# Kernel optimization log

Hardware: AMD Instinct MI355X
Metric: run time of the kernel (lower is better)

Reference implementation:

```python
import jax, jax.numpy as jnp
import numpy as np

N, M = 16384, 12
OA, OB = 92, 41
AF, BF = 128, 64
LD, NC, B = 2, 3, 128


def _bn(x, g, b):
    # training-mode BatchNorm1d over all leading dims (biased variance), eps=1e-5
    x2 = x.reshape(-1, x.shape[-1])
    m = x2.mean(0)
    v = x2.var(0)
    return (x - m) * jax.lax.rsqrt(v + 1e-5) * g + b


def _conv(atom, nbr, idx, Wa, Wb, g1a, b1a, g1b, b1b, g2a, b2a):
    n, m = idx.shape
    # gather neighbor atom features and concat [self, neighbor, bond] -> [N,M,2A+Bf]
    total = jnp.concatenate([jnp.broadcast_to(atom[:, None, :], (n, m, atom.shape[1])), atom[idx], nbr], axis=2)
    ga = _bn(jnp.einsum('nmi,io->nmo', total, Wa), g1a, b1a)
    af, ac = jnp.split(ga, 2, axis=2)
    asum = _bn(jnp.sum(jax.nn.sigmoid(af) * jax.nn.softplus(ac), axis=1), g2a, b2a)
    out1 = jax.nn.softplus(atom + asum)
    gb = _bn(jnp.einsum('nmi,io->nmo', total, Wb), g1b, b1b)
    bf, bc = jnp.split(gb, 2, axis=2)
    out2 = jax.nn.softplus(nbr + jax.nn.sigmoid(bf) * jax.nn.softplus(bc))
    return out1, out2


def _forward(atom_fea, nbr_fea, emb_atom_W, emb_atom_b, emb_bond_W, emb_bond_b,
             emb_atom2_W, emb_atom2_b, emb_bond2_W, emb_bond2_b,
             mu_W, mu_b, logvar_W, logvar_b, dec_W, dec_b,
             c1_Wa, c1_Wb, c1_g1a, c1_b1a, c1_g1b, c1_b1b, c1_g2a, c1_b2a,
             c2_Wa, c2_Wb, c2_g1a, c2_b1a, c2_g1b, c2_b1b, c2_g2a, c2_b2a,
             nbr_fea_idx, num_crystals):
    n, m = nbr_fea_idx.shape
    a_per = n // num_crystals
    anbr = atom_fea[nbr_fea_idx]  # [N,M,OA]
    total_input_fea = jnp.concatenate([jnp.broadcast_to(atom_fea[:, None, :], anbr.shape), anbr, nbr_fea], axis=2)
    a = atom_fea @ emb_atom_W + emb_atom_b            # [N,AF]
    nb = nbr_fea @ emb_bond_W + emb_bond_b            # [N,M,BF]
    for i in range(NC):
        a, nb = _conv(a, nb, nbr_fea_idx, c1_Wa[i], c1_Wb[i], c1_g1a[i], c1_b1a[i], c1_g1b[i], c1_b1b[i], c1_g2a[i], c1_b2a[i])
    non_pooled = jnp.concatenate([a, nb.reshape(n, -1)], axis=1)  # [N, AF+M*BF]
    # equal-size contiguous crystals -> pooling = reshape + mean
    pa = jax.nn.softplus(a.reshape(num_crystals, a_per, -1).mean(1))
    pn = jax.nn.softplus(nb.reshape(num_crystals, a_per, m, -1).mean(1)).reshape(num_crystals, -1)
    pooled = jnp.concatenate([pa, pn], axis=1)        # [B, AF+M*BF]
    mu = pooled @ mu_W + mu_b
    logvar = pooled @ logvar_W + logvar_b
    eps = jax.random.normal(jax.random.key(42), mu.shape, mu.dtype)  # fixed reparam noise
    z = mu + eps * jnp.exp(0.5 * logvar)
    zd = z @ dec_W + dec_b                            # [B, AF+M*BF]
    dec = jax.nn.softplus((non_pooled.reshape(num_crystals, a_per, -1) * zd[:, None, :] / pooled[:, None, :]).reshape(n, -1))
    za = dec[:, :AF]
    dn = dec[:, AF:].reshape(n, m, BF)
    for i in range(NC):
        za, dn = _conv(za, dn, nbr_fea_idx, c2_Wa[i], c2_Wb[i], c2_g1a[i], c2_b1a[i], c2_g1b[i], c2_b1b[i], c2_g2a[i], c2_b2a[i])
    za = jax.nn.sigmoid(za @ emb_atom2_W + emb_atom2_b)   # [N,OA]
    dn = jax.nn.sigmoid(dn @ emb_bond2_W + emb_bond2_b)   # [N,M,OB]
    znbr = za[nbr_fea_idx]
    z_dec = jnp.concatenate([jnp.broadcast_to(za[:, None, :], znbr.shape), znbr, dn], axis=2)  # [N,M,2*OA+OB]
    return z_dec, mu, logvar, z, total_input_fea


def setup_inputs() -> dict:
    key = jax.random.key(0)
    def nrm(i, shape, s=0.05):
        return (jax.random.normal(jax.random.fold_in(key, i), shape) * s).astype(jnp.float32)
    inp = {
        'atom_fea': nrm(0, (N, OA), 1.0),
        'nbr_fea': nrm(1, (N, M, OB), 1.0),
        'nbr_fea_idx': jax.random.randint(jax.random.fold_in(key, 2), (N, M), 0, N),
        'num_crystals': B,
        'emb_atom_W': nrm(3, (OA, AF)), 'emb_atom_b': jnp.zeros((AF,), jnp.float32),
        'emb_bond_W': nrm(4, (OB, BF)), 'emb_bond_b': jnp.zeros((BF,), jnp.float32),
        'emb_atom2_W': nrm(5, (AF, OA)), 'emb_atom2_b': jnp.zeros((OA,), jnp.float32),
        'emb_bond2_W': nrm(6, (BF, OB)), 'emb_bond2_b': jnp.zeros((OB,), jnp.float32),
        'mu_W': nrm(7, (AF + M * BF, LD)), 'mu_b': jnp.zeros((LD,), jnp.float32),
        'logvar_W': nrm(8, (AF + M * BF, LD)), 'logvar_b': jnp.zeros((LD,), jnp.float32),
        'dec_W': nrm(9, (LD, AF + M * BF)), 'dec_b': jnp.zeros((AF + M * BF,), jnp.float32),
        'c1_Wa': nrm(10, (NC, 2 * AF + BF, 2 * AF)), 'c1_Wb': nrm(11, (NC, 2 * AF + BF, 2 * BF)),
        'c1_g1a': jnp.ones((NC, 2 * AF), jnp.float32), 'c1_b1a': jnp.zeros((NC, 2 * AF), jnp.float32),
        'c1_g1b': jnp.ones((NC, 2 * BF), jnp.float32), 'c1_b1b': jnp.zeros((NC, 2 * BF), jnp.float32),
        'c1_g2a': jnp.ones((NC, AF), jnp.float32), 'c1_b2a': jnp.zeros((NC, AF), jnp.float32),
        'c2_Wa': nrm(12, (NC, 2 * AF + BF, 2 * AF)), 'c2_Wb': nrm(13, (NC, 2 * AF + BF, 2 * BF)),
        'c2_g1a': jnp.ones((NC, 2 * AF), jnp.float32), 'c2_b1a': jnp.zeros((NC, 2 * AF), jnp.float32),
        'c2_g1b': jnp.ones((NC, 2 * BF), jnp.float32), 'c2_b1b': jnp.zeros((NC, 2 * BF), jnp.float32),
        'c2_g2a': jnp.ones((NC, AF), jnp.float32), 'c2_b2a': jnp.zeros((NC, AF), jnp.float32),
    }
    return inp


def reference(atom_fea, nbr_fea, nbr_fea_idx, num_crystals,
              emb_atom_W, emb_atom_b, emb_bond_W, emb_bond_b,
              emb_atom2_W, emb_atom2_b, emb_bond2_W, emb_bond2_b,
              mu_W, mu_b, logvar_W, logvar_b, dec_W, dec_b,
              c1_Wa, c1_Wb, c1_g1a, c1_b1a, c1_g1b, c1_b1b, c1_g2a, c1_b2a,
              c2_Wa, c2_Wb, c2_g1a, c2_b1a, c2_g1b, c2_b1b, c2_g2a, c2_b2a):
    return _forward(atom_fea, nbr_fea, emb_atom_W, emb_atom_b, emb_bond_W, emb_bond_b,
                    emb_atom2_W, emb_atom2_b, emb_bond2_W, emb_bond2_b,
                    mu_W, mu_b, logvar_W, logvar_b, dec_W, dec_b,
                    c1_Wa, c1_Wb, c1_g1a, c1_b1a, c1_g1b, c1_b1b, c1_g2a, c1_b2a,
                    c2_Wa, c2_Wb, c2_g1a, c2_b1a, c2_g1b, c2_b1b, c2_g2a, c2_b2a,
                    nbr_fea_idx, num_crystals)
```

## Files before the change

kernel.cpp:

```cpp
#include <hip/hip_runtime.h>
#include <hip/hip_bf16.h>
#include <hip/hip_fp16.h>
#include <cstdint>
#include <cstddef>

#define N_ATOM 16384
#define M_NBR  12
#define NCRY   128
#define NM     (N_ATOM*M_NBR)

#define O_ZDEC 0
#define O_MU   44236800
#define O_LV   44237056
#define O_Z    44237312
#define O_TIF  44237568

typedef unsigned short ushort_t;
typedef float f32x4 __attribute__((ext_vector_type(4)));
typedef short bf16x8 __attribute__((ext_vector_type(8)));
typedef unsigned int u32x4 __attribute__((ext_vector_type(4)));

__device__ __forceinline__ float sigmoidf_(float x){
  return __fdividef(1.f, 1.f + __expf(-x));
}
__device__ __forceinline__ float softplusf_(float x){
  return fmaxf(x,0.f) + 0.69314718056f * __log2f(1.f + __expf(-fabsf(x)));
}
__device__ __forceinline__ uint32_t rotl32_(uint32_t x, int r){ return (x<<r)|(x>>(32-r)); }
__device__ __forceinline__ float bf2f(ushort_t u){ return __uint_as_float(((uint32_t)u)<<16); }
__device__ __forceinline__ ushort_t f2bf(float x){
  uint32_t u = __float_as_uint(x);
  uint32_t r = (u + 0x7FFFu + ((u>>16)&1u)) >> 16;
  return (ushort_t)r;
}

#define GLDS16(g, l) __builtin_amdgcn_global_load_lds( \
    (const __attribute__((address_space(1))) void*)(g), \
    (__attribute__((address_space(3))) void*)(l), 16, 0, 0)

__global__ void gen_eps_kernel(float* __restrict__ eps){
  int j = threadIdx.x;
  const uint32_t k0 = 0u, k1 = 42u;
  const uint32_t ks2 = k0 ^ k1 ^ 0x1BD11BDAu;
  uint32_t x0 = 0u + k0;
  uint32_t x1 = (uint32_t)j + k1;
#define RND_(r) { x0 += x1; x1 = rotl32_(x1, r); x1 ^= x0; }
  RND_(13) RND_(15) RND_(26) RND_(6)  x0 += k1;  x1 += ks2 + 1u;
  RND_(17) RND_(29) RND_(16) RND_(24) x0 += ks2; x1 += k0 + 2u;
  RND_(13) RND_(15) RND_(26) RND_(6)  x0 += k0;  x1 += k1 + 3u;
  RND_(17) RND_(29) RND_(16) RND_(24) x0 += k1;  x1 += ks2 + 4u;
  RND_(13) RND_(15) RND_(26) RND_(6)  x0 += ks2; x1 += k0 + 5u;
#undef RND_
  uint32_t bits = x0 ^ x1;
  float f = __uint_as_float((bits >> 9) | 0x3f800000u) - 1.0f;
  float u = __fadd_rn(__fmul_rn(f, 1.99999994f), -0.99999994f);
  u = fmaxf(-0.99999994f, u);
  float w = -log1pf(-u*u);
  float p;
  if (w < 5.0f){
    w -= 2.5f;
    p = 2.81022636e-08f;
    p = fmaf(p, w, 3.43273939e-07f);
    p = fmaf(p, w, -3.5233877e-06f);
    p = fmaf(p, w, -4.39150654e-06f);
    p = fmaf(p, w, 0.00021858087f);
    p = fmaf(p, w, -0.00125372503f);
    p = fmaf(p, w, -0.00417768164f);
    p = fmaf(p, w, 0.246640727f);
    p = fmaf(p, w, 1.50140941f);
  } else {
    w = sqrtf(w) - 3.0f;
    p = -0.000200214257f;
    p = fmaf(p, w, 0.000100950558f);
    p = fmaf(p, w, 0.00134934322f);
    p = fmaf(p, w, -0.00367342844f);
    p = fmaf(p, w, 0.00573950773f);
    p = fmaf(p, w, -0.0076224613f);
    p = fmaf(p, w, 0.00943887047f);
    p = fmaf(p, w, 1.00167406f);
    p = fmaf(p, w, 2.83297682f);
  }
  eps[j] = 1.41421356237f * (p * u);
}

__global__ void tif_v2(const float* __restrict__ atom, const float* __restrict__ nbr,
                       const int* __restrict__ idx, float* __restrict__ out){
  int e0 = blockIdx.x*2048 + threadIdx.x;
#pragma unroll
  for (int i=0;i<8;++i){
    int e = e0 + i*256;
    int r = e/225, c = e - r*225;
    float v;
    if (c < 92)       v = atom[(r/12)*92 + c];
    else if (c < 184) v = atom[idx[r]*92 + (c-92)];
    else              v = nbr[(size_t)r*41 + (c-184)];
    __builtin_nontemporal_store(v, out + (size_t)e);
  }
}

__global__ void embed_atom_kernel(const float* __restrict__ atom, const float* __restrict__ W,
                                  const float* __restrict__ bias, ushort_t* __restrict__ a0){
  __shared__ float row[92];
  int i = blockIdx.x; int t = threadIdx.x;
  if (t < 92) row[t] = atom[i*92+t];
  __syncthreads();
  float s = bias[t];
#pragma unroll
  for (int k=0;k<92;++k) s = fmaf(row[k], W[k*128+t], s);
  a0[(size_t)i*128+t] = f2bf(s);
}

__global__ void embed_bond_kernel(const float* __restrict__ nbr, const float* __restrict__ W,
                                  const float* __restrict__ bias, ushort_t* __restrict__ nb0){
  __shared__ float rows[4][41];
  int r0 = blockIdx.x*4; int t = threadIdx.x;
  if (t < 164) rows[t/41][t%41] = nbr[(size_t)r0*41 + t];
  __syncthreads();
  int rr = t >> 6, c = t & 63;
  float s = bias[c];
#pragma unroll
  for (int k=0;k<41;++k) s = fmaf(rows[rr][k], W[k*64+c], s);
  nb0[(size_t)(r0+rr)*64 + c] = f2bf(s);
}

__global__ void wtr2_kernel(const float* __restrict__ Wa, const float* __restrict__ Wb,
                            ushort_t* __restrict__ Wt, float* __restrict__ zstats){
  __shared__ ushort_t tile[32][33];
  if (blockIdx.x == 0 && blockIdx.y == 0){
#pragma unroll
    for (int k=0;k<4;++k) zstats[threadIdx.x + k*256] = 0.f;
  }
  int by = blockIdx.y;
  const float* W; int NO, o0, obase;
  if (by < 8){ W = Wa; NO = 256; o0 = by*32; obase = o0; }
  else       { W = Wb; NO = 128; o0 = (by-8)*32; obase = 256 + o0; }
  int k0 = blockIdx.x*32;
  int tx = threadIdx.x & 31, ty = threadIdx.x >> 5;
#pragma unroll
  for (int i = ty; i < 32; i += 8)
    tile[i][tx] = f2bf(W[(size_t)(k0+i)*NO + o0 + tx]);
  __syncthreads();
#pragma unroll
  for (int i = ty; i < 32; i += 8)
    Wt[(size_t)(obase+i)*320 + k0 + tx] = tile[tx][i];
}

#define GEMM_LDS_V9 75776
__launch_bounds__(256, 2)
__global__ void conv_gemm_v9(const ushort_t* __restrict__ a_bf, const ushort_t* __restrict__ nb_bf,
                             const int* __restrict__ idx, const ushort_t* __restrict__ Wt,
                             __half* __restrict__ O, float* __restrict__ sums){
  extern __shared__ char smraw[];
  ushort_t* sm   = (ushort_t*)smraw;
  float*   sqred = (float*)(smraw + 73728);
  int*     idxs  = (int*)(smraw + 74752);
  ushort_t* As = sm;
  ushort_t* Bs = sm + 24576;
  const int t = threadIdx.x;
  const int lane = t & 63;
  const int w = t >> 6;
  const int lm = lane & 15, lg = lane >> 4;
  const int row0 = blockIdx.x * 256;
  const int cb   = blockIdx.y;
  const int col0 = cb * 128;
  __half* Ob = O + (size_t)cb * ((size_t)NM*128);

  idxs[t] = idx[row0 + t];
  sqred[t] = 0.f;

  auto stage = [&](int ks, int b_){
    ushort_t* Ad = As + b_*8192;
    ushort_t* Bd = Bs + b_*4096;
#pragma unroll
    for (int i=0;i<4;++i){
      int e = t + i*256;
      int r = e >> 2, ch = e & 3;
      const ushort_t* ga;
      if (ks < 4)      ga = a_bf + (size_t)((row0+r)/12)*128 + ks*32 + ch*8;
      else if (ks < 8) ga = a_bf + (size_t)idxs[r]*128 + (ks-4)*32 + ch*8;
      else             ga = nb_bf + (size_t)(row0+r)*64 + (ks-8)*32 + ch*8;
      GLDS16(ga, Ad + e*8);
    }
#pragma unroll
    for (int i=0;i<2;++i){
      int e = t + i*256;
      int r = e >> 2, ch = e & 3;
      GLDS16(Wt + (size_t)(col0+r)*320 + ks*32 + ch*8, Bd + e*8);
    }
  };

  stage(0, 0);
  stage(1, 1);

  f32x4 acc[4][8] = {};
#pragma unroll
  for (int ks = 0; ks < 10; ++ks){
    const int buf = ks % 3;
    if (ks < 8){
      stage(ks+2, (ks+2) % 3);
      asm volatile("s_waitcnt vmcnt(12)" ::: "memory");
    } else if (ks == 8){
      asm volatile("s_waitcnt vmcnt(6)" ::: "memory");
    } else {
      asm volatile("s_waitcnt vmcnt(0)" ::: "memory");
    }
    __builtin_amdgcn_s_barrier();
    __builtin_amdgcn_sched_barrier(0);
    const ushort_t* Ab = As + buf*8192;
    const ushort_t* Bb = Bs + buf*4096;
    bf16x8 afr[4], bfr[8];
#pragma unroll
    for (int fm=0; fm<4; ++fm)
      afr[fm] = *(const bf16x8*)&Ab[(w*64 + fm*16 + lm)*32 + lg*8];
#pragma unroll
    for (int fn=0; fn<8; ++fn)
      bfr[fn] = *(const bf16x8*)&Bb[(fn*16 + lm)*32 + lg*8];
    __builtin_amdgcn_s_setprio(1);
#pragma unroll
    for (int fm=0; fm<4; ++fm)
#pragma unroll
      for (int fn=0; fn<8; ++fn)
        acc[fm][fn] = __builtin_amdgcn_mfma_f32_16x16x32_bf16(afr[fm], bfr[fn], acc[fm][fn], 0, 0, 0);
    __builtin_amdgcn_s_setprio(0);
    asm volatile("s_waitcnt lgkmcnt(0)" ::: "memory");
    __builtin_amdgcn_sched_barrier(0);
    __builtin_amdgcn_s_barrier();
  }

#pragma unroll
  for (int fm=0; fm<4; ++fm){
    int rw = w*64 + fm*16 + lg*4;
#pragma unroll
    for (int fn=0; fn<8; ++fn){
      int cl = fn*16 + lm;
#pragma unroll
      for (int j=0; j<4; ++j){
        __half h = __float2half(acc[fm][fn][j]);
        sm[(rw+j)*136 + cl] = *(ushort_t*)&h;
      }
    }
  }
  __syncthreads();

  const int cch = t & 15, rb = t >> 4;
  float s1[8] = {0.f,0.f,0.f,0.f,0.f,0.f,0.f,0.f};
  float s2[8] = {0.f,0.f,0.f,0.f,0.f,0.f,0.f,0.f};
#pragma unroll
  for (int i=0; i<16; ++i){
    int row = rb + i*16;
    u32x4 v = *(const u32x4*)&sm[row*136 + cch*8];
    __builtin_nontemporal_store(v, (u32x4*)(Ob + (size_t)(row0+row)*128 + cch*8));
    const __half* hp = (const __half*)&v;
#pragma unroll
    for (int k=0;k<8;++k){
      float f = __half2float(hp[k]);
      s1[k] += f;
      s2[k] += f*f;
    }
  }
#pragma unroll
  for (int k=0;k<8;++k){
    atomicAdd(&sqred[cch*8+k], s1[k]);
    atomicAdd(&sqred[128+cch*8+k], s2[k]);
  }
  __syncthreads();
  if (t < 128){
    atomicAdd(&sums[col0 + t], sqred[t]);
    atomicAdd(&sums[384 + col0 + t], sqred[128+t]);
  }
}

__global__ void apply_gagb(const __half* __restrict__ O0, const __half* __restrict__ O1,
                           const __half* __restrict__ O2, ushort_t* __restrict__ nb,
                           const float* __restrict__ sums,
                           const float* __restrict__ g1a, const float* __restrict__ b1a,
                           const float* __restrict__ g1b, const float* __restrict__ b1b,
                           float* __restrict__ asum, float* __restrict__ st){
  __shared__ float red[256];
  int bx = blockIdx.x;
  int t = threadIdx.x;
  if (bx < 1024){
    red[t] = 0.f;
    int c8 = t & 15, al = t >> 4;
    int i = bx*16 + al;
    int c0 = c8*8;
    float gf[8], bfv[8], gc[8], bcv[8];
#pragma unroll
    for (int k=0;k<8;++k){
      int c = c0+k;
      float mf = sums[c]*(1.f/NM);
      float rf = rsqrtf(sums[384+c]*(1.f/NM) - mf*mf + 1e-5f);
      gf[k]  = g1a[c]*rf;      bfv[k] = b1a[c] - mf*gf[k];
      float mc = sums[c+128]*(1.f/NM);
      float rc = rsqrtf(sums[384+c+128]*(1.f/NM) - mc*mc + 1e-5f);
      gc[k]  = g1a[c+128]*rc;  bcv[k] = b1a[c+128] - mc*gc[k];
    }
    float s[8] = {0.f,0.f,0.f,0.f,0.f,0.f,0.f,0.f};
    size_t base = (size_t)i*12*128;
#pragma unroll
    for (int j=0;j<12;++j){
      u32x4 vf = __builtin_nontemporal_load((const u32x4*)(O0 + base + j*128 + c0));
      u32x4 vc = __builtin_nontemporal_load((const u32x4*)(O1 + base + j*128 + c0));
      const __half* hf = (const __half*)&vf;
      const __half* hc = (const __half*)&vc;
#pragma unroll
      for (int k=0;k<8;++k)
        s[k] += sigmoidf_(fmaf(__half2float(hf[k]), gf[k], bfv[k]))
              * softplusf_(fmaf(__half2float(hc[k]), gc[k], bcv[k]));
    }
    float* dst = asum + (size_t)i*128 + c0;
    __syncthreads();
#pragma unroll
    for (int k=0;k<8;++k){
      dst[k] = s[k];
      atomicAdd(&red[c0+k], s[k]);
      atomicAdd(&red[128+c0+k], s[k]*s[k]);
    }
    __syncthreads();
    atomicAdd(&st[t], red[t]);
  } else {
    int c8 = t & 7, rloc = t >> 3;
    int r = (bx-1024)*32 + rloc;
    int c0 = c8*8;
    float gf[8], bfv[8], gc[8], bcv[8];
#pragma unroll
    for (int k=0;k<8;++k){
      int c = c0+k;
      float mf = sums[256+c]*(1.f/NM);
      float rf = rsqrtf(sums[384+256+c]*(1.f/NM) - mf*mf + 1e-5f);
      gf[k]  = g1b[c]*rf;      bfv[k] = b1b[c] - mf*gf[k];
      float mc = sums[256+64+c]*(1.f/NM);
      float rc = rsqrtf(sums[384+256+64+c]*(1.f/NM) - mc*mc + 1e-5f);
      gc[k]  = g1b[c+64]*rc;   bcv[k] = b1b[c+64] - mc*gc[k];
    }
    size_t gbase = (size_t)r*128;
    u32x4 vf = __builtin_nontemporal_load((const u32x4*)(O2 + gbase + c0));
    u32x4 vc = __builtin_nontemporal_load((const u32x4*)(O2 + gbase + 64 + c0));
    const __half* hf = (const __half*)&vf;
    const __half* hc = (const __half*)&vc;
    ushort_t* np = nb + (size_t)r*64 + c0;
    u32x4 old = *(const u32x4*)np;
    const ushort_t* op = (const ushort_t*)&old;
    u32x4 outv;
    ushort_t* ov = (ushort_t*)&outv;
#pragma unroll
    for (int k=0;k<8;++k){
      float x = bf2f(op[k]) + sigmoidf_(fmaf(__half2float(hf[k]), gf[k], bfv[k]))
                            * softplusf_(fmaf(__half2float(hc[k]), gc[k], bcv[k]));
      ov[k] = f2bf(softplusf_(x));
    }
    *(u32x4*)np = outv;
  }
}

__global__ void out1_wtr(ushort_t* __restrict__ a0, const float* __restrict__ asum,
                         const float* __restrict__ st, const float* __restrict__ g2a,
                         const float* __restrict__ b2a,
                         const float* __restrict__ Wa_next, const float* __restrict__ Wb_next,
                         ushort_t* __restrict__ Wt, float* __restrict__ zstats){
  __shared__ ushort_t tile[32][33];
  int bx = blockIdx.x;
  int t = threadIdx.x;
  if (bx < 120){
    if (Wa_next == nullptr) return;
    int by = bx / 10, kx = bx - by*10;
    const float* W; int NO, o0, obase;
    if (by < 8){ W = Wa_next; NO = 256; o0 = by*32; obase = o0; }
    else       { W = Wb_next; NO = 128; o0 = (by-8)*32; obase = 256 + o0; }
    int k0 = kx*32;
    int tx = t & 31, ty = t >> 5;
#pragma unroll
    for (int i = ty; i < 32; i += 8)
      tile[i][tx] = f2bf(W[(size_t)(k0+i)*NO + o0 + tx]);
    __syncthreads();
#pragma unroll
    for (int i = ty; i < 32; i += 8)
      Wt[(size_t)(obase+i)*320 + k0 + tx] = tile[tx][i];
  } else if (bx == 120){
    if (Wa_next == nullptr) return;
#pragma unroll
    for (int k=0;k<4;++k) zstats[t + k*256] = 0.f;
  } else {
    int e = (bx-121)*256 + t;
    int c = e & 127;
    float m  = st[c]*(1.f/N_ATOM);
    float var = st[128+c]*(1.f/N_ATOM) - m*m;
    float rs = rsqrtf(var + 1e-5f);
    float g = g2a[c]*rs;
    float b = b2a[c] - m*g;
    a0[e] = f2bf(softplusf_(bf2f(a0[e]) + fmaf(asum[e], g, b)));
  }
}

__global__ void pool_a_kernel(const ushort_t* __restrict__ a, float* __restrict__ pooled){
  int b = blockIdx.x; int c = threadIdx.x;
  float s = 0.f;
  for (int i=0;i<128;++i) s += bf2f(a[(size_t)((b<<7)+i)*128 + c]);
  pooled[b*896 + c] = softplusf_(s * (1.f/128.f));
}

__launch_bounds__(768)
__global__ void pool_n_kernel(const ushort_t* __restrict__ nb, float* __restrict__ pooled){
  int b = blockIdx.x; int t = threadIdx.x;
  float s = 0.f;
  for (int i=0;i<128;++i) s += bf2f(nb[(size_t)((b<<7)+i)*768 + t]);
  pooled[b*896 + 128 + t] = softplusf_(s * (1.f/128.f));
}

__global__ void muz_kernel(const float* __restrict__ pooled, const float* __restrict__ muW,
                           const float* __restrict__ mub, const float* __restrict__ lvW,
                           const float* __restrict__ lvb, const float* __restrict__ eps,
                           float* __restrict__ out_mu, float* __restrict__ out_lv,
                           float* __restrict__ out_z, float* __restrict__ zws){
  int t = threadIdx.x;
  int b = t >> 1, l = t & 1;
  const float* pr = pooled + b*896;
  float smu = mub[l], slv = lvb[l];
  for (int k=0;k<896;++k){
    float p = pr[k];
    smu = fmaf(p, muW[k*2+l], smu);
    slv = fmaf(p, lvW[k*2+l], slv);
  }
  out_mu[t] = smu; out_lv[t] = slv;
  float zv = fmaf(eps[t], __expf(0.5f*slv), smu);
  out_z[t] = zv; zws[t] = zv;
}

__global__ void compute_f_kernel(const float* __restrict__ zws, const float* __restrict__ decW,
                                 const float* __restrict__ decb, const float* __restrict__ pooled,
                                 float* __restrict__ f){
  int b = blockIdx.x;
  float z0 = zws[b*2], z1 = zws[b*2+1];
  for (int k = threadIdx.x; k < 896; k += 256){
    float zd = fmaf(z0, decW[k], fmaf(z1, decW[896+k], decb[k]));
    f[b*896+k] = __fdividef(zd, pooled[b*896+k]);
  }
}

__global__ void dec_atom_kernel(ushort_t* __restrict__ a, const float* __restrict__ f){
  int e = blockIdx.x*256+threadIdx.x;
  int c = e & 127; int b = e >> 14;
  a[e] = f2bf(softplusf_(bf2f(a[e]) * f[b*896 + c]));
}

__global__ void dec_bond_kernel(ushort_t* __restrict__ nb, const float* __restrict__ f){
  int i = blockIdx.x; int off = blockIdx.y*256 + threadIdx.x;
  int b = i >> 7;
  size_t e = (size_t)i*768 + off;
  nb[e] = f2bf(softplusf_(bf2f(nb[e]) * f[b*896 + 128 + off]));
}

__global__ void embed_atom2_kernel(const ushort_t* __restrict__ a, const float* __restrict__ W,
                                   const float* __restrict__ bias, float* __restrict__ za2){
  __shared__ float row[128];
  int i = blockIdx.x; int t = threadIdx.x;
  row[t] = bf2f(a[(size_t)i*128+t]);
  __syncthreads();
  if (t < 92){
    float s = bias[t];
#pragma unroll
    for (int k=0;k<128;++k) s = fmaf(row[k], W[k*92+t], s);
    za2[(size_t)i*92+t] = sigmoidf_(s);
  }
}

__global__ void bproj_kernel(const ushort_t* __restrict__ nb, const float* __restrict__ W,
                             const float* __restrict__ bias, float* __restrict__ bp){
  __shared__ float Ws[64][41];
  __shared__ float rows[6][64];
  int t = threadIdx.x;
  for (int e=t; e<64*41; e+=256) Ws[e/41][e%41] = W[e];
  int r0 = blockIdx.x*6;
  for (int e=t; e<6*64; e+=256){
    int rr = e>>6, c = e&63;
    rows[rr][c] = bf2f(nb[(size_t)(r0+rr)*64 + c]);
  }
  __syncthreads();
  if (t < 246){
    int rr = t/41, o = t - rr*41;
    float s = bias[o];
#pragma unroll
    for (int k=0;k<64;++k) s = fmaf(rows[rr][k], Ws[k][o], s);
    bp[(size_t)(r0+rr)*41 + o] = sigmoidf_(s);
  }
}

__global__ void zdec_v2(const float* __restrict__ za2, const float* __restrict__ bp,
                        const int* __restrict__ idx, float* __restrict__ out){
  int e0 = blockIdx.x*2048 + threadIdx.x;
#pragma unroll
  for (int i=0;i<8;++i){
    int e = e0 + i*256;
    int r = e/225, c = e - r*225;
    float v;
    if (c < 92)       v = za2[(size_t)(r/12)*92 + c];
    else if (c < 184) v = za2[(size_t)idx[r]*92 + (c-92)];
    else              v = bp[(size_t)r*41 + (c-184)];
    __builtin_nontemporal_store(v, out + (size_t)e);
  }
}

struct WsPlan {
  ushort_t *Abf, *NBbf, *Wt;
  __half* big;
  float *asum, *pooled, *fbuf, *zws, *eps, *sums0, *sums1;
};

struct PassW {
  const float *Wa,*Wb,*g1a,*b1a,*g1b,*b1b,*g2a,*b2a;
};

extern "C" void kernel_launch(void* const* d_in, const int* in_sizes, int n_in,
                              void* d_out, int out_size, void* d_ws, size_t ws_size,
                              hipStream_t stream) {
  (void)in_sizes; (void)n_in; (void)out_size; (void)ws_size;
  const float* atom_fea   = (const float*)d_in[0];
  const float* nbr_fea    = (const float*)d_in[1];
  const int*   idx        = (const int*)d_in[2];
  const float* emb_atom_W = (const float*)d_in[4];
  const float* emb_atom_b = (const float*)d_in[5];
  const float* emb_bond_W = (const float*)d_in[6];
  const float* emb_bond_b = (const float*)d_in[7];
  const float* emb_atom2_W= (const float*)d_in[8];
  const float* emb_atom2_b= (const float*)d_in[9];
  const float* emb_bond2_W= (const float*)d_in[10];
  const float* emb_bond2_b= (const float*)d_in[11];
  const float* mu_W       = (const float*)d_in[12];
  const float* mu_b       = (const float*)d_in[13];
  const float* lv_W       = (const float*)d_in[14];
  const float* lv_b       = (const float*)d_in[15];
  const float* dec_W      = (const float*)d_in[16];
  const float* dec_b      = (const float*)d_in[17];
  const float* c1_Wa  = (const float*)d_in[18];
  const float* c1_Wb  = (const float*)d_in[19];
  const float* c1_g1a = (const float*)d_in[20];
  const float* c1_b1a = (const float*)d_in[21];
  const float* c1_g1b = (const float*)d_in[22];
  const float* c1_b1b = (const float*)d_in[23];
  const float* c1_g2a = (const float*)d_in[24];
  const float* c1_b2a = (const float*)d_in[25];
  const float* c2_Wa  = (const float*)d_in[26];
  const float* c2_Wb  = (const float*)d_in[27];
  const float* c2_g1a = (const float*)d_in[28];
  const float* c2_b1a = (const float*)d_in[29];
  const float* c2_g1b = (const float*)d_in[30];
  const float* c2_b1b = (const float*)d_in[31];
  const float* c2_g2a = (const float*)d_in[32];
  const float* c2_b2a = (const float*)d_in[33];

  float* out = (float*)d_out;

  hipFuncSetAttribute((const void*)conv_gemm_v9,
                      hipFuncAttributeMaxDynamicSharedMemorySize, GEMM_LDS_V9);

  WsPlan P;
  char* w = (char*)d_ws;
  auto alloc = [&](size_t bytes) -> char* {
    char* p = w; w += (bytes + 255) & ~(size_t)255; return p;
  };
  P.Abf    = (ushort_t*)alloc((size_t)N_ATOM*128*2);
  P.NBbf   = (ushort_t*)alloc((size_t)NM*64*2);
  P.big    = (__half*)  alloc((size_t)NM*384*2);
  P.asum   = (float*)   alloc((size_t)N_ATOM*128*4);
  P.pooled = (float*)   alloc(114688*4);
  P.fbuf   = (float*)   alloc(114688*4);
  P.Wt     = (ushort_t*)alloc(384*320*2);
  P.zws    = (float*)   alloc(256*4);
  P.eps    = (float*)   alloc(256*4);
  P.sums0  = (float*)   alloc(1024*4);
  P.sums1  = (float*)   alloc(1024*4);
  float* za2   = P.asum;
  float* bproj = (float*)P.big;

  PassW pw[6] = {
    { c1_Wa,            c1_Wb,            c1_g1a,       c1_b1a,       c1_g1b,       c1_b1b,       c1_g2a,       c1_b2a       },
    { c1_Wa+320*256,    c1_Wb+320*128,    c1_g1a+256,   c1_b1a+256,   c1_g1b+128,   c1_b1b+128,   c1_g2a+128,   c1_b2a+128   },
    { c1_Wa+2*320*256,  c1_Wb+2*320*128,  c1_g1a+2*256, c1_b1a+2*256, c1_g1b+2*128, c1_b1b+2*128, c1_g2a+2*128, c1_b2a+2*128 },
    { c2_Wa,            c2_Wb,            c2_g1a,       c2_b1a,       c2_g1b,       c2_b1b,       c2_g2a,       c2_b2a       },
    { c2_Wa+320*256,    c2_Wb+320*128,    c2_g1a+256,   c2_b1a+256,   c2_g1b+128,   c2_b1b+128,   c2_g2a+128,   c2_b2a+128   },
    { c2_Wa+2*320*256,  c2_Wb+2*320*128,  c2_g1a+2*256, c2_b1a+2*256, c2_g1b+2*128, c2_b1b+2*128, c2_g2a+2*128, c2_b2a+2*128 },
  };

  auto conv_pass = [&](int p){
    float* sums_cur = (p & 1) ? P.sums1 : P.sums0;
    float* sums_nxt = (p & 1) ? P.sums0 : P.sums1;
    const __half* O0 = P.big;
    const __half* O1 = P.big + (size_t)NM*128;
    const __half* O2 = P.big + (size_t)NM*256;
    conv_gemm_v9<<<dim3(NM/256, 3), 256, GEMM_LDS_V9, stream>>>(P.Abf, P.NBbf, idx, P.Wt, P.big, sums_cur);
    apply_gagb<<<7168, 256, 0, stream>>>(O0, O1, O2, P.NBbf, sums_cur,
                                         pw[p].g1a, pw[p].b1a, pw[p].g1b, pw[p].b1b,
                                         P.asum, sums_cur + 768);
    const float* Wa_n = (p < 5) ? pw[p+1].Wa : nullptr;
    const float* Wb_n = (p < 5) ? pw[p+1].Wb : nullptr;
    out1_wtr<<<8313, 256, 0, stream>>>(P.Abf, P.asum, sums_cur + 768,
                                       pw[p].g2a, pw[p].b2a, Wa_n, Wb_n, P.Wt, sums_nxt);
  };

  gen_eps_kernel<<<1, 256, 0, stream>>>(P.eps);
  tif_v2<<<21600, 256, 0, stream>>>(atom_fea, nbr_fea, idx, out + O_TIF);
  embed_atom_kernel<<<N_ATOM, 128, 0, stream>>>(atom_fea, emb_atom_W, emb_atom_b, P.Abf);
  embed_bond_kernel<<<NM/4, 256, 0, stream>>>(nbr_fea, emb_bond_W, emb_bond_b, P.NBbf);
  wtr2_kernel<<<dim3(10,12), 256, 0, stream>>>(pw[0].Wa, pw[0].Wb, P.Wt, P.sums0);

  conv_pass(0);
  conv_pass(1);
  conv_pass(2);

  pool_a_kernel<<<NCRY, 128, 0, stream>>>(P.Abf, P.pooled);
  pool_n_kernel<<<NCRY, 768, 0, stream>>>(P.NBbf, P.pooled);
  muz_kernel<<<1, 256, 0, stream>>>(P.pooled, mu_W, mu_b, lv_W, lv_b, P.eps,
                                    out + O_MU, out + O_LV, out + O_Z, P.zws);
  compute_f_kernel<<<NCRY, 256, 0, stream>>>(P.zws, dec_W, dec_b, P.pooled, P.fbuf);
  dec_atom_kernel<<<N_ATOM*128/256, 256, 0, stream>>>(P.Abf, P.fbuf);
  dim3 gdb(N_ATOM, 3);
  dec_bond_kernel<<<gdb, 256, 0, stream>>>(P.NBbf, P.fbuf);

  conv_pass(3);
  conv_pass(4);
  conv_pass(5);

  embed_atom2_kernel<<<N_ATOM, 128, 0, stream>>>(P.Abf, emb_atom2_W, emb_atom2_b, za2);
  bproj_kernel<<<NM/6, 256, 0, stream>>>(P.NBbf, emb_bond2_W, emb_bond2_b, bproj);
  zdec_v2<<<21600, 256, 0, stream>>>(za2, bproj, idx, out + O_ZDEC);
}
```

Before: 1.630 ms.

## Merge small launches and swizzle GEMM workgroup order for cache locality

Several independent small kernels are merged into single launches that branch on block index: atom and bond embedding, the two pooling kernels, and the two decoder scaling kernels. The eps generation is folded into the mu/z kernel. The conv GEMM moves from a 2D grid to a flat grid with a remapping that spreads consecutive workgroups across 8 groups, so row-tile/column-block pairs interleave differently. The aim is to cut launch overhead and improve L2 reuse of gathered rows. The remapping changes cache behaviour in ways that are hard to predict.

```diff
diff --git a/kernel.cpp b/kernel.cpp
--- a/kernel.cpp
+++ b/kernel.cpp
@@ -37,51 +37,6 @@
 #define GLDS16(g, l) __builtin_amdgcn_global_load_lds( \
     (const __attribute__((address_space(1))) void*)(g), \
     (__attribute__((address_space(3))) void*)(l), 16, 0, 0)
-
-__global__ void gen_eps_kernel(float* __restrict__ eps){
-  int j = threadIdx.x;
-  const uint32_t k0 = 0u, k1 = 42u;
-  const uint32_t ks2 = k0 ^ k1 ^ 0x1BD11BDAu;
-  uint32_t x0 = 0u + k0;
-  uint32_t x1 = (uint32_t)j + k1;
-#define RND_(r) { x0 += x1; x1 = rotl32_(x1, r); x1 ^= x0; }
-  RND_(13) RND_(15) RND_(26) RND_(6)  x0 += k1;  x1 += ks2 + 1u;
-  RND_(17) RND_(29) RND_(16) RND_(24) x0 += ks2; x1 += k0 + 2u;
-  RND_(13) RND_(15) RND_(26) RND_(6)  x0 += k0;  x1 += k1 + 3u;
-  RND_(17) RND_(29) RND_(16) RND_(24) x0 += k1;  x1 += ks2 + 4u;
-  RND_(13) RND_(15) RND_(26) RND_(6)  x0 += ks2; x1 += k0 + 5u;
-#undef RND_
-  uint32_t bits = x0 ^ x1;
-  float f = __uint_as_float((bits >> 9) | 0x3f800000u) - 1.0f;
-  float u = __fadd_rn(__fmul_rn(f, 1.99999994f), -0.99999994f);
-  u = fmaxf(-0.99999994f, u);
-  float w = -log1pf(-u*u);
-  float p;
-  if (w < 5.0f){
-    w -= 2.5f;
-    p = 2.81022636e-08f;
-    p = fmaf(p, w, 3.43273939e-07f);
-    p = fmaf(p, w, -3.5233877e-06f);
-    p = fmaf(p, w, -4.39150654e-06f);
-    p = fmaf(p, w, 0.00021858087f);
-    p = fmaf(p, w, -0.00125372503f);
-    p = fmaf(p, w, -0.00417768164f);
-    p = fmaf(p, w, 0.246640727f);
-    p = fmaf(p, w, 1.50140941f);
-  } else {
-    w = sqrtf(w) - 3.0f;
-    p = -0.000200214257f;
-    p = fmaf(p, w, 0.000100950558f);
-    p = fmaf(p, w, 0.00134934322f);
-    p = fmaf(p, w, -0.00367342844f);
-    p = fmaf(p, w, 0.00573950773f);
-    p = fmaf(p, w, -0.0076224613f);
-    p = fmaf(p, w, 0.00943887047f);
-    p = fmaf(p, w, 1.00167406f);
-    p = fmaf(p, w, 2.83297682f);
-  }
-  eps[j] = 1.41421356237f * (p * u);
-}
 
 __global__ void tif_v2(const float* __restrict__ atom, const float* __restrict__ nbr,
                        const int* __restrict__ idx, float* __restrict__ out){
@@ -98,29 +53,32 @@
   }
 }
 
-__global__ void embed_atom_kernel(const float* __restrict__ atom, const float* __restrict__ W,
-                                  const float* __restrict__ bias, ushort_t* __restrict__ a0){
-  __shared__ float row[92];
-  int i = blockIdx.x; int t = threadIdx.x;
-  if (t < 92) row[t] = atom[i*92+t];
-  __syncthreads();
-  float s = bias[t];
-#pragma unroll
-  for (int k=0;k<92;++k) s = fmaf(row[k], W[k*128+t], s);
-  a0[(size_t)i*128+t] = f2bf(s);
-}
-
-__global__ void embed_bond_kernel(const float* __restrict__ nbr, const float* __restrict__ W,
-                                  const float* __restrict__ bias, ushort_t* __restrict__ nb0){
-  __shared__ float rows[4][41];
-  int r0 = blockIdx.x*4; int t = threadIdx.x;
-  if (t < 164) rows[t/41][t%41] = nbr[(size_t)r0*41 + t];
-  __syncthreads();
-  int rr = t >> 6, c = t & 63;
-  float s = bias[c];
-#pragma unroll
-  for (int k=0;k<41;++k) s = fmaf(rows[rr][k], W[k*64+c], s);
-  nb0[(size_t)(r0+rr)*64 + c] = f2bf(s);
+__global__ void embed_fused(const float* __restrict__ atom, const float* __restrict__ nbr,
+                            const float* __restrict__ Wa, const float* __restrict__ ba,
+                            const float* __restrict__ Wb, const float* __restrict__ bb,
+                            ushort_t* __restrict__ a0, ushort_t* __restrict__ nb0){
+  int bx = blockIdx.x; int t = threadIdx.x;
+  if (bx < 8192){
+    __shared__ float row[2][92];
+    int al = t >> 7, tt = t & 127;
+    int i = bx*2 + al;
+    if (tt < 92) row[al][tt] = atom[i*92+tt];
+    __syncthreads();
+    float s = ba[tt];
+#pragma unroll
+    for (int k=0;k<92;++k) s = fmaf(row[al][k], Wa[k*128+tt], s);
+    a0[(size_t)i*128+tt] = f2bf(s);
+  } else {
+    __shared__ float rows[4][41];
+    int r0 = (bx-8192)*4;
+    if (t < 164) rows[t/41][t%41] = nbr[(size_t)r0*41 + t];
+    __syncthreads();
+    int rr = t >> 6, c = t & 63;
+    float s = bb[c];
+#pragma unroll
+    for (int k=0;k<41;++k) s = fmaf(rows[rr][k], Wb[k*64+c], s);
+    nb0[(size_t)(r0+rr)*64 + c] = f2bf(s);
+  }
 }
 
 __global__ void wtr2_kernel(const float* __restrict__ Wa, const float* __restrict__ Wb,
@@ -147,9 +105,9 @@
 
 #define GEMM_LDS_V9 75776
 __launch_bounds__(256, 2)
-__global__ void conv_gemm_v9(const ushort_t* __restrict__ a_bf, const ushort_t* __restrict__ nb_bf,
-                             const int* __restrict__ idx, const ushort_t* __restrict__ Wt,
-                             __half* __restrict__ O, float* __restrict__ sums){
+__global__ void conv_gemm_v10(const ushort_t* __restrict__ a_bf, const ushort_t* __restrict__ nb_bf,
+                              const int* __restrict__ idx, const ushort_t* __restrict__ Wt,
+                              __half* __restrict__ O, float* __restrict__ sums){
   extern __shared__ char smraw[];
   ushort_t* sm   = (ushort_t*)smraw;
   float*   sqred = (float*)(smraw + 73728);
@@ -160,8 +118,11 @@
   const int lane = t & 63;
   const int w = t >> 6;
   const int lm = lane & 15, lg = lane >> 4;
-  const int row0 = blockIdx.x * 256;
-  const int cb   = blockIdx.y;
+  const int flat = blockIdx.x;
+  const int wg   = (flat & 7)*288 + (flat >> 3);
+  const int r0i  = wg / 3;
+  const int cb   = wg - r0i*3;
+  const int row0 = r0i * 256;
   const int col0 = cb * 128;
   __half* Ob = O + (size_t)cb * ((size_t)NM*128);
 
@@ -392,27 +353,84 @@
   }
 }
 
-__global__ void pool_a_kernel(const ushort_t* __restrict__ a, float* __restrict__ pooled){
-  int b = blockIdx.x; int c = threadIdx.x;
-  float s = 0.f;
-  for (int i=0;i<128;++i) s += bf2f(a[(size_t)((b<<7)+i)*128 + c]);
-  pooled[b*896 + c] = softplusf_(s * (1.f/128.f));
-}
-
-__launch_bounds__(768)
-__global__ void pool_n_kernel(const ushort_t* __restrict__ nb, float* __restrict__ pooled){
-  int b = blockIdx.x; int t = threadIdx.x;
-  float s = 0.f;
-  for (int i=0;i<128;++i) s += bf2f(nb[(size_t)((b<<7)+i)*768 + t]);
-  pooled[b*896 + 128 + t] = softplusf_(s * (1.f/128.f));
-}
-
-__global__ void muz_kernel(const float* __restrict__ pooled, const float* __restrict__ muW,
-                           const float* __restrict__ mub, const float* __restrict__ lvW,
-                           const float* __restrict__ lvb, const float* __restrict__ eps,
-                           float* __restrict__ out_mu, float* __restrict__ out_lv,
-                           float* __restrict__ out_z, float* __restrict__ zws){
+__global__ void pool_fused(const ushort_t* __restrict__ a, const ushort_t* __restrict__ nb,
+                           float* __restrict__ pooled){
+  __shared__ float sh[256];
+  int bx = blockIdx.x; int t = threadIdx.x;
+  if (bx < 128){
+    int b = bx;
+    int c = t & 127, h = t >> 7;
+    float s = 0.f;
+    for (int i=h;i<128;i+=2) s += bf2f(a[(size_t)((b<<7)+i)*128 + c]);
+    sh[t] = s;
+    __syncthreads();
+    if (t < 128)
+      pooled[b*896 + t] = softplusf_((sh[t]+sh[t+128]) * (1.f/128.f));
+  } else {
+    int b = bx - 128;
+    float s0=0.f, s1=0.f, s2=0.f;
+    for (int i=0;i<128;++i){
+      size_t base = (size_t)((b<<7)+i)*768;
+      s0 += bf2f(nb[base + t]);
+      s1 += bf2f(nb[base + t + 256]);
+      s2 += bf2f(nb[base + t + 512]);
+    }
+    pooled[b*896 + 128 + t]       = softplusf_(s0 * (1.f/128.f));
+    pooled[b*896 + 128 + t + 256] = softplusf_(s1 * (1.f/128.f));
+    pooled[b*896 + 128 + t + 512] = softplusf_(s2 * (1.f/128.f));
+  }
+}
+
+__global__ void muz_v2(const float* __restrict__ pooled, const float* __restrict__ muW,
+                       const float* __restrict__ mub, const float* __restrict__ lvW,
+                       const float* __restrict__ lvb,
+                       float* __restrict__ out_mu, float* __restrict__ out_lv,
+                       float* __restrict__ out_z, float* __restrict__ zws){
   int t = threadIdx.x;
+  float epsv;
+  {
+    const uint32_t k0 = 0u, k1 = 42u;
+    const uint32_t ks2 = k0 ^ k1 ^ 0x1BD11BDAu;
+    uint32_t x0 = 0u + k0;
+    uint32_t x1 = (uint32_t)t + k1;
+#define RND_(r) { x0 += x1; x1 = rotl32_(x1, r); x1 ^= x0; }
+    RND_(13) RND_(15) RND_(26) RND_(6)  x0 += k1;  x1 += ks2 + 1u;
+    RND_(17) RND_(29) RND_(16) RND_(24) x0 += ks2; x1 += k0 + 2u;
+    RND_(13) RND_(15) RND_(26) RND_(6)  x0 += k0;  x1 += k1 + 3u;
+    RND_(17) RND_(29) RND_(16) RND_(24) x0 += k1;  x1 += ks2 + 4u;
+    RND_(13) RND_(15) RND_(26) RND_(6)  x0 += ks2; x1 += k0 + 5u;
+#undef RND_
+    uint32_t bits = x0 ^ x1;
+    float f = __uint_as_float((bits >> 9) | 0x3f800000u) - 1.0f;
+    float u = __fadd_rn(__fmul_rn(f, 1.99999994f), -0.99999994f);
+    u = fmaxf(-0.99999994f, u);
+    float w = -log1pf(-u*u);
+    float p;
+    if (w < 5.0f){
+      w -= 2.5f;
+      p = 2.81022636e-08f;
+      p = fmaf(p, w, 3.43273939e-07f);
+      p = fmaf(p, w, -3.5233877e-06f);
+      p = fmaf(p, w, -4.39150654e-06f);
+      p = fmaf(p, w, 0.00021858087f);
+      p = fmaf(p, w, -0.00125372503f);
+      p = fmaf(p, w, -0.00417768164f);
+      p = fmaf(p, w, 0.246640727f);
+      p = fmaf(p, w, 1.50140941f);
+    } else {
+      w = sqrtf(w) - 3.0f;
+      p = -0.000200214257f;
+      p = fmaf(p, w, 0.000100950558f);
+      p = fmaf(p, w, 0.00134934322f);
+      p = fmaf(p, w, -0.00367342844f);
+      p = fmaf(p, w, 0.00573950773f);
+      p = fmaf(p, w, -0.0076224613f);
+      p = fmaf(p, w, 0.00943887047f);
+      p = fmaf(p, w, 1.00167406f);
+      p = fmaf(p, w, 2.83297682f);
+    }
+    epsv = 1.41421356237f * (p * u);
+  }
   int b = t >> 1, l = t & 1;
   const float* pr = pooled + b*896;
   float smu = mub[l], slv = lvb[l];
@@ -422,7 +440,7 @@
     slv = fmaf(p, lvW[k*2+l], slv);
   }
   out_mu[t] = smu; out_lv[t] = slv;
-  float zv = fmaf(eps[t], __expf(0.5f*slv), smu);
+  float zv = fmaf(epsv, __expf(0.5f*slv), smu);
   out_z[t] = zv; zws[t] = zv;
 }
 
@@ -437,17 +455,21 @@
   }
 }
 
-__global__ void dec_atom_kernel(ushort_t* __restrict__ a, const float* __restrict__ f){
-  int e = blockIdx.x*256+threadIdx.x;
-  int c = e & 127; int b = e >> 14;
-  a[e] = f2bf(softplusf_(bf2f(a[e]) * f[b*896 + c]));
-}
-
-__global__ void dec_bond_kernel(ushort_t* __restrict__ nb, const float* __restrict__ f){
-  int i = blockIdx.x; int off = blockIdx.y*256 + threadIdx.x;
-  int b = i >> 7;
-  size_t e = (size_t)i*768 + off;
-  nb[e] = f2bf(softplusf_(bf2f(nb[e]) * f[b*896 + 128 + off]));
+__global__ void dec_fused(ushort_t* __restrict__ a, ushort_t* __restrict__ nb,
+                          const float* __restrict__ f){
+  int bx = blockIdx.x; int t = threadIdx.x;
+  if (bx < 8192){
+    int e = bx*256 + t;
+    int c = e & 127; int b = e >> 14;
+    a[e] = f2bf(softplusf_(bf2f(a[e]) * f[b*896 + c]));
+  } else {
+    int blk = bx - 8192;
+    int oy = blk >> 14, i = blk & 16383;
+    int off = oy*256 + t;
+    int b = i >> 7;
+    size_t e = (size_t)i*768 + off;
+    nb[e] = f2bf(softplusf_(bf2f(nb[e]) * f[b*896 + 128 + off]));
+  }
 }
 
 __global__ void embed_atom2_kernel(const ushort_t* __restrict__ a, const float* __restrict__ W,
@@ -503,7 +525,7 @@
 struct WsPlan {
   ushort_t *Abf, *NBbf, *Wt;
   __half* big;
-  float *asum, *pooled, *fbuf, *zws, *eps, *sums0, *sums1;
+  float *asum, *pooled, *fbuf, *zws, *sums0, *sums1;
 };
 
 struct PassW {
@@ -550,7 +572,7 @@
 
   float* out = (float*)d_out;
 
-  hipFuncSetAttribute((const void*)conv_gemm_v9,
+  hipFuncSetAttribute((const void*)conv_gemm_v10,
                       hipFuncAttributeMaxDynamicSharedMemorySize, GEMM_LDS_V9);
 
   WsPlan P;
@@ -566,7 +588,6 @@
   P.fbuf   = (float*)   alloc(114688*4);
   P.Wt     = (ushort_t*)alloc(384*320*2);
   P.zws    = (float*)   alloc(256*4);
-  P.eps    = (float*)   alloc(256*4);
   P.sums0  = (float*)   alloc(1024*4);
   P.sums1  = (float*)   alloc(1024*4);
   float* za2   = P.asum;
@@ -587,7 +608,7 @@
     const __half* O0 = P.big;
     const __half* O1 = P.big + (size_t)NM*128;
     const __half* O2 = P.big + (size_t)NM*256;
-    conv_gemm_v9<<<dim3(NM/256, 3), 256, GEMM_LDS_V9, stream>>>(P.Abf, P.NBbf, idx, P.Wt, P.big, sums_cur);
+    conv_gemm_v10<<<2304, 256, GEMM_LDS_V9, stream>>>(P.Abf, P.NBbf, idx, P.Wt, P.big, sums_cur);
     apply_gagb<<<7168, 256, 0, stream>>>(O0, O1, O2, P.NBbf, sums_cur,
                                          pw[p].g1a, pw[p].b1a, pw[p].g1b, pw[p].b1b,
                                          P.asum, sums_cur + 768);
@@ -597,24 +618,20 @@
                                        pw[p].g2a, pw[p].b2a, Wa_n, Wb_n, P.Wt, sums_nxt);
   };
 
-  gen_eps_kernel<<<1, 256, 0, stream>>>(P.eps);
   tif_v2<<<21600, 256, 0, stream>>>(atom_fea, nbr_fea, idx, out + O_TIF);
-  embed_atom_kernel<<<N_ATOM, 128, 0, stream>>>(atom_fea, emb_atom_W, emb_atom_b, P.Abf);
-  embed_bond_kernel<<<NM/4, 256, 0, stream>>>(nbr_fea, emb_bond_W, emb_bond_b, P.NBbf);
+  embed_fused<<<57344, 256, 0, stream>>>(atom_fea, nbr_fea, emb_atom_W, emb_atom_b,
+                                         emb_bond_W, emb_bond_b, P.Abf, P.NBbf);
   wtr2_kernel<<<dim3(10,12), 256, 0, stream>>>(pw[0].Wa, pw[0].Wb, P.Wt, P.sums0);
 
   conv_pass(0);
   conv_pass(1);
   conv_pass(2);
 
-  pool_a_kernel<<<NCRY, 128, 0, stream>>>(P.Abf, P.pooled);
-  pool_n_kernel<<<NCRY, 768, 0, stream>>>(P.NBbf, P.pooled);
-  muz_kernel<<<1, 256, 0, stream>>>(P.pooled, mu_W, mu_b, lv_W, lv_b, P.eps,
-                                    out + O_MU, out + O_LV, out + O_Z, P.zws);
+  pool_fused<<<256, 256, 0, stream>>>(P.Abf, P.NBbf, P.pooled);
+  muz_v2<<<1, 256, 0, stream>>>(P.pooled, mu_W, mu_b, lv_W, lv_b,
+                                out + O_MU, out + O_LV, out + O_Z, P.zws);
   compute_f_kernel<<<NCRY, 256, 0, stream>>>(P.zws, dec_W, dec_b, P.pooled, P.fbuf);
-  dec_atom_kernel<<<N_ATOM*128/256, 256, 0, stream>>>(P.Abf, P.fbuf);
-  dim3 gdb(N_ATOM, 3);
-  dec_bond_kernel<<<gdb, 256, 0, stream>>>(P.NBbf, P.fbuf);
+  dec_fused<<<57344, 256, 0, stream>>>(P.Abf, P.NBbf, P.fbuf);
 
   conv_pass(3);
   conv_pass(4);
```

After: 1.584 ms. 2.9% less time.
